# Optimization experiments

Measured on AMD Instinct MI355X. Metric: run time of the kernel, lower is better.

## Reference

```python
import jax, jax.numpy as jnp
import numpy as np

D_MODEL = 1024
N_HEADS = 16
D_HEAD = D_MODEL // N_HEADS  # 64
SCALE = 1.0 / float(np.sqrt(D_HEAD))


def setup_inputs() -> dict:
    key = jax.random.key(0)
    kx, kq, kk, kv, ko = jax.random.split(key, 5)
    B, L = 1, 4096
    x = jax.random.normal(kx, (B, L, D_MODEL), dtype=jnp.float32)
    init = 0.02  # small init so softmax isn't saturated
    Wq = jax.random.normal(kq, (D_MODEL, D_MODEL), dtype=jnp.float32) * init
    Wk = jax.random.normal(kk, (D_MODEL, D_MODEL), dtype=jnp.float32) * init
    Wv = jax.random.normal(kv, (D_MODEL, D_MODEL), dtype=jnp.float32) * init
    Wo = jax.random.normal(ko, (D_MODEL, D_MODEL), dtype=jnp.float32) * init
    return {"x": x, "Wq": Wq, "Wk": Wk, "Wv": Wv, "Wo": Wo}


def reference(x, Wq, Wk, Wv, Wo):
    # x: [B, L, d_model]; torch Linear (no bias): y = x @ W.T
    B, L, _ = x.shape

    def split_heads(t):  # [B, L, d_model] -> [B, H, L, Dh]
        return t.reshape(B, L, N_HEADS, D_HEAD).transpose(0, 2, 1, 3)

    q = split_heads(x @ Wq.T)
    k = split_heads(x @ Wk.T)
    v = split_heads(x @ Wv.T)

    # Full (non-flash) attention: explicit [B, H, L, L] scores (causal=False, eval dropout=0)
    scores = jnp.einsum("bhld,bhmd->bhlm", q, k) * SCALE
    attn = jax.nn.softmax(scores, axis=-1)
    out = jnp.einsum("bhlm,bhmd->bhld", attn, v)

    out = out.transpose(0, 2, 1, 3).reshape(B, L, D_MODEL)
    return out @ Wo.T
```

## Files before the change

### kernel.cpp

```cpp
#include <hip/hip_runtime.h>

typedef _Float16 f16_t;
typedef __fp16 fp16x2 __attribute__((ext_vector_type(2)));
typedef _Float16 f16x2 __attribute__((ext_vector_type(2)));
typedef _Float16 f16x4 __attribute__((ext_vector_type(4)));
typedef _Float16 f16x8 __attribute__((ext_vector_type(8)));
typedef float f32x4 __attribute__((ext_vector_type(4)));

#define D_MODEL 1024
#define LSEQ 4096
#define NH 16
#define DH 64
#define QSCALE 0.18033688011112042f

#define GLDS16(g, l)                                                     \
    __builtin_amdgcn_global_load_lds(                                    \
        (const __attribute__((address_space(1))) void*)(g),              \
        (__attribute__((address_space(3))) void*)(l), 16, 0, 0)

#define WAIT_VM(n) asm volatile("s_waitcnt vmcnt(" #n ")" ::: "memory")

__global__ __launch_bounds__(256) void cvt_all(const float* __restrict__ x,
                                               const float* __restrict__ w0,
                                               const float* __restrict__ w1,
                                               const float* __restrict__ w2,
                                               const float* __restrict__ w3,
                                               f16_t* __restrict__ xb,
                                               f16_t* __restrict__ wq) {
    const int id = blockIdx.x;
    const float* src;
    f16_t* dst;
    float scale = 1.f;
    int i;
    if (id < 4096) {
        src = x; dst = xb;
        i = (id * 256 + threadIdx.x) * 4;
    } else {
        const int r = id - 4096;
        const int q = r >> 10;
        src = (q == 0) ? w0 : (q == 1) ? w1 : (q == 2) ? w2 : w3;
        if (q == 0) scale = QSCALE;
        dst = wq + (size_t)q * (D_MODEL * D_MODEL);
        i = ((r & 1023) * 256 + threadIdx.x) * 4;
    }
    float4 v = *(const float4*)&src[i];
    alignas(8) f16_t o4[4] = {(f16_t)(v.x * scale), (f16_t)(v.y * scale),
                              (f16_t)(v.z * scale), (f16_t)(v.w * scale)};
    *(uint2*)&dst[i] = *(const uint2*)o4;
}

__global__ __launch_bounds__(256, 3) void gemm_f16(const f16_t* __restrict__ A,
                                                   const f16_t* __restrict__ B,
                                                   void* __restrict__ Cout,
                                                   int M, int N, int K, int mode) {
    __shared__ alignas(16) f16_t As[3][128 * 32];
    __shared__ alignas(16) f16_t Bs[3][128 * 32];

    const int tid  = threadIdx.x;
    const int wave = tid >> 6;
    const int lane = tid & 63;
    const int quad = lane >> 4;
    const int l16  = lane & 15;
    const int wm = (wave & 1) * 64;
    const int wn = (wave >> 1) * 64;

    const int gx  = gridDim.x;
    const int gy  = gridDim.y;
    const int lid = blockIdx.y * gx + blockIdx.x;
    const int xcd = lid & 7;
    const int sub = lid >> 3;
    const int bm  = (xcd * (gx >> 3) + sub / gy) * 128;
    const int bn  = (sub % gy) * 128;

    f32x4 acc[4][4] = {};
    const int nk = K / 32;

    auto stage = [&](int kt, int b) {
        const int c0 = wave * 2;
        GLDS16(&A[(size_t)(bm + c0 * 16 + l16) * K + kt * 32 + quad * 8],
               &As[b][c0 * 512]);
        GLDS16(&A[(size_t)(bm + (c0 + 1) * 16 + l16) * K + kt * 32 + quad * 8],
               &As[b][(c0 + 1) * 512]);
        GLDS16(&B[(size_t)(bn + c0 * 16 + l16) * K + kt * 32 + quad * 8],
               &Bs[b][c0 * 512]);
        GLDS16(&B[(size_t)(bn + (c0 + 1) * 16 + l16) * K + kt * 32 + quad * 8],
               &Bs[b][(c0 + 1) * 512]);
    };

    stage(0, 0);
    stage(1, 1);
    for (int kt = 0; kt < nk; ++kt) {
        const int cb = kt % 3;
        if (kt < nk - 1) WAIT_VM(4);
        else             WAIT_VM(0);
        __syncthreads();
        if (kt + 2 < nk) stage(kt + 2, (kt + 2) % 3);

        f16x8 af[4], bfr[4];
#pragma unroll
        for (int mt = 0; mt < 4; ++mt)
            af[mt] = *(const f16x8*)&As[cb][((wm >> 4) + mt) * 512 + lane * 8];
#pragma unroll
        for (int nt = 0; nt < 4; ++nt)
            bfr[nt] = *(const f16x8*)&Bs[cb][((wn >> 4) + nt) * 512 + lane * 8];
#pragma unroll
        for (int mt = 0; mt < 4; ++mt)
#pragma unroll
            for (int nt = 0; nt < 4; ++nt)
                acc[mt][nt] = __builtin_amdgcn_mfma_f32_16x16x32_f16(
                    bfr[nt], af[mt], acc[mt][nt], 0, 0, 0);
    }

#pragma unroll
    for (int mt = 0; mt < 4; ++mt)
#pragma unroll
        for (int nt = 0; nt < 4; ++nt) {
            int row = bm + wm + mt * 16 + l16;
            int col = bn + wn + nt * 16 + quad * 4;
            if (mode == 0) {
                f16x4 p = {(f16_t)acc[mt][nt][0], (f16_t)acc[mt][nt][1],
                           (f16_t)acc[mt][nt][2], (f16_t)acc[mt][nt][3]};
                *(f16x4*)&((f16_t*)Cout)[((size_t)(col >> 6) * M + row) * 64 +
                                         (col & 63)] = p;
            } else {
                *(f32x4*)&((float*)Cout)[(size_t)row * N + col] = acc[mt][nt];
            }
        }
}

__global__ __launch_bounds__(256) void transpose_v(const f16_t* __restrict__ vh,
                                                   f16_t* __restrict__ v4) {
    __shared__ f16_t Ts[64][72];
    const int t = threadIdx.x;
    const int lt = blockIdx.x;
    const int head = blockIdx.y;

#pragma unroll
    for (int i = 0; i < 2; ++i) {
        int idx = t + i * 256;
        int row = idx >> 3, part = idx & 7;
        *(uint4*)&Ts[row][part * 8] =
            *(const uint4*)&vh[((size_t)head * LSEQ + lt * 64 + row) * DH + part * 8];
    }
    __syncthreads();

    const int c8  = t >> 5;
    const int mtp = c8 >> 2, dt = c8 & 3;
    const int l0  = (t & 31) * 2;
    alignas(16) f16_t buf[16];
#pragma unroll
    for (int li = 0; li < 2; ++li) {
        const int l = l0 + li;
        const int g = l >> 4, l16 = l & 15;
#pragma unroll
        for (int j = 0; j < 8; ++j) {
            int key = mtp * 32 + (j < 4 ? 4 * g + j : 16 + 4 * g + (j - 4));
            buf[li * 8 + j] = Ts[key][dt * 16 + l16];
        }
    }
    f16_t* dst = v4 + (size_t)head * (LSEQ * DH) + (size_t)lt * 4096 + c8 * 512 + l0 * 8;
    *(uint4*)&dst[0] = *(const uint4*)&buf[0];
    *(uint4*)&dst[8] = *(const uint4*)&buf[8];
}

__global__ __launch_bounds__(512, 4) void attn_kernel(const f16_t* __restrict__ qh,
                                                      const f16_t* __restrict__ kh,
                                                      const f16_t* __restrict__ v4,
                                                      f16_t* __restrict__ ao) {
    __shared__ alignas(16) f16_t smem[32768];
    __shared__ alignas(16) float lscr[8 * 64];
    f16_t* KsB = smem;
    f16_t* VsB = smem + 16384;

    const int tid  = threadIdx.x;
    const int wave = tid >> 6;
    const int lane = tid & 63;
    const int quad = lane >> 4;
    const int l16  = lane & 15;
    const int wq   = wave & 3;
    const int kha  = wave >> 2;

    const int id = blockIdx.x;
    const int head = id & 15;
    const int qrow0 = (id >> 4) * 128 + wq * 32;

    const f16_t* Q  = qh + (size_t)head * LSEQ * DH;
    const f16_t* K  = kh + (size_t)head * LSEQ * DH;
    const f16_t* V4 = v4 + (size_t)head * (LSEQ * DH);

    f16x8 qf[2][2];
#pragma unroll
    for (int qt = 0; qt < 2; ++qt)
#pragma unroll
        for (int kc = 0; kc < 2; ++kc)
            qf[qt][kc] = *(const f16x8*)
                &Q[(size_t)(qrow0 + qt * 16 + l16) * DH + kc * 32 + quad * 8];

    f32x4 o[4][2] = {};
    float lp[2] = {0.f, 0.f};

    auto stage = [&](int kt, int b) {
        f16_t* ks = KsB + (kha * 2 + b) * 4096;
        f16_t* vs = VsB + (kha * 2 + b) * 4096;
        const int ktg = kha * 32 + kt;
#pragma unroll
        for (int jj = 0; jj < 2; ++jj) {
            const int j = wq * 2 + jj;
            GLDS16(&K[(size_t)(ktg * 64 + wq * 16 + l16) * DH + jj * 32 + quad * 8],
                   &ks[j * 512]);
            GLDS16(&V4[(size_t)ktg * 4096 + wq * 1024 + jj * 512 + lane * 8],
                   &vs[wq * 1024 + jj * 512]);
        }
    };

    const int NT = LSEQ / 2 / 64;
    stage(0, 0);
    for (int kt = 0; kt < NT; ++kt) {
        const int cb = kt & 1;
        WAIT_VM(0);
        __syncthreads();
        if (kt + 1 < NT) stage(kt + 1, cb ^ 1);

        const f16_t* ks = KsB + (kha * 2 + cb) * 4096;
        const f16_t* vs = VsB + (kha * 2 + cb) * 4096;

        f32x4 sA[2][2] = {};
        {
            f16x8 kfA[4];
#pragma unroll
            for (int c = 0; c < 4; ++c)
                kfA[c] = *(const f16x8*)&ks[c * 512 + lane * 8];
#pragma unroll
            for (int h = 0; h < 2; ++h)
#pragma unroll
                for (int qt = 0; qt < 2; ++qt) {
                    sA[h][qt] = __builtin_amdgcn_mfma_f32_16x16x32_f16(
                        kfA[h * 2 + 0], qf[qt][0], sA[h][qt], 0, 0, 0);
                    sA[h][qt] = __builtin_amdgcn_mfma_f32_16x16x32_f16(
                        kfA[h * 2 + 1], qf[qt][1], sA[h][qt], 0, 0, 0);
                }
        }
        f32x4 sB[2][2] = {};
        {
            f16x8 kfB[4];
#pragma unroll
            for (int c = 0; c < 4; ++c)
                kfB[c] = *(const f16x8*)&ks[(4 + c) * 512 + lane * 8];
#pragma unroll
            for (int h = 0; h < 2; ++h)
#pragma unroll
                for (int qt = 0; qt < 2; ++qt) {
                    sB[h][qt] = __builtin_amdgcn_mfma_f32_16x16x32_f16(
                        kfB[h * 2 + 0], qf[qt][0], sB[h][qt], 0, 0, 0);
                    sB[h][qt] = __builtin_amdgcn_mfma_f32_16x16x32_f16(
                        kfB[h * 2 + 1], qf[qt][1], sB[h][qt], 0, 0, 0);
                }
        }

#pragma unroll
        for (int mtp = 0; mtp < 2; ++mtp) {
            f32x4 (*s)[2] = (mtp == 0) ? sA : sB;

            f16x8 vfd[4];
#pragma unroll
            for (int dt = 0; dt < 4; ++dt)
                vfd[dt] = *(const f16x8*)&vs[(mtp * 4 + dt) * 512 + lane * 8];

#pragma unroll
            for (int qt = 0; qt < 2; ++qt) {
                float e0 = __builtin_amdgcn_exp2f(s[0][qt][0]);
                float e1 = __builtin_amdgcn_exp2f(s[0][qt][1]);
                float e2 = __builtin_amdgcn_exp2f(s[0][qt][2]);
                float e3 = __builtin_amdgcn_exp2f(s[0][qt][3]);
                float e4 = __builtin_amdgcn_exp2f(s[1][qt][0]);
                float e5 = __builtin_amdgcn_exp2f(s[1][qt][1]);
                float e6 = __builtin_amdgcn_exp2f(s[1][qt][2]);
                float e7 = __builtin_amdgcn_exp2f(s[1][qt][3]);
                lp[qt] += ((e0 + e1) + (e2 + e3)) + ((e4 + e5) + (e6 + e7));
                fp16x2 p01 = __builtin_amdgcn_cvt_pkrtz(e0, e1);
                fp16x2 p23 = __builtin_amdgcn_cvt_pkrtz(e2, e3);
                fp16x2 p45 = __builtin_amdgcn_cvt_pkrtz(e4, e5);
                fp16x2 p67 = __builtin_amdgcn_cvt_pkrtz(e6, e7);
                f16x8 p = {__builtin_bit_cast(f16x2, p01)[0],
                           __builtin_bit_cast(f16x2, p01)[1],
                           __builtin_bit_cast(f16x2, p23)[0],
                           __builtin_bit_cast(f16x2, p23)[1],
                           __builtin_bit_cast(f16x2, p45)[0],
                           __builtin_bit_cast(f16x2, p45)[1],
                           __builtin_bit_cast(f16x2, p67)[0],
                           __builtin_bit_cast(f16x2, p67)[1]};
#pragma unroll
                for (int dt = 0; dt < 4; ++dt)
                    o[dt][qt] = __builtin_amdgcn_mfma_f32_16x16x32_f16(
                        vfd[dt], p, o[dt][qt], 0, 0, 0);
            }
        }
    }

    __syncthreads();
    float* scr = (float*)smem;
    if (wave >= 4) {
#pragma unroll
        for (int dt = 0; dt < 4; ++dt)
#pragma unroll
            for (int qt = 0; qt < 2; ++qt)
                *(f32x4*)&scr[(((wave - 4) * 8 + dt * 2 + qt) * 64 + lane) * 4] =
                    o[dt][qt];
#pragma unroll
        for (int qt = 0; qt < 2; ++qt)
            lscr[((wave - 4) * 2 + qt) * 64 + lane] = lp[qt];
    }
    __syncthreads();
    if (wave < 4) {
#pragma unroll
        for (int dt = 0; dt < 4; ++dt)
#pragma unroll
            for (int qt = 0; qt < 2; ++qt)
                o[dt][qt] += *(const f32x4*)
                    &scr[((wave * 8 + dt * 2 + qt) * 64 + lane) * 4];
#pragma unroll
        for (int qt = 0; qt < 2; ++qt) {
            float t = lp[qt] + lscr[(wave * 2 + qt) * 64 + lane];
            t += __shfl_xor(t, 16, 64);
            t += __shfl_xor(t, 32, 64);
            lp[qt] = 1.f / t;
        }
#pragma unroll
        for (int dt = 0; dt < 4; ++dt)
#pragma unroll
            for (int qt = 0; qt < 2; ++qt) {
                f16x4 ov = {(f16_t)(o[dt][qt][0] * lp[qt]),
                            (f16_t)(o[dt][qt][1] * lp[qt]),
                            (f16_t)(o[dt][qt][2] * lp[qt]),
                            (f16_t)(o[dt][qt][3] * lp[qt])};
                int qrow = qrow0 + qt * 16 + l16;
                *(f16x4*)&ao[(size_t)qrow * D_MODEL + head * 64 + dt * 16 +
                             quad * 4] = ov;
            }
    }
}

extern "C" void kernel_launch(void* const* d_in, const int* in_sizes, int n_in,
                              void* d_out, int out_size, void* d_ws, size_t ws_size,
                              hipStream_t stream) {
    const float* x  = (const float*)d_in[0];
    const float* Wq = (const float*)d_in[1];
    const float* Wk = (const float*)d_in[2];
    const float* Wv = (const float*)d_in[3];
    const float* Wo = (const float*)d_in[4];

    f16_t* xb = (f16_t*)d_ws;
    f16_t* wq = xb + (size_t)LSEQ * D_MODEL;
    f16_t* wo = wq + (size_t)3 * D_MODEL * D_MODEL;
    f16_t* qh = wo + (size_t)D_MODEL * D_MODEL;
    f16_t* kh = qh + (size_t)LSEQ * D_MODEL;
    f16_t* vh = kh + (size_t)LSEQ * D_MODEL;
    f16_t* v4 = vh + (size_t)LSEQ * D_MODEL;
    f16_t* ao = v4 + (size_t)LSEQ * D_MODEL;

    cvt_all<<<4096 + 4 * 1024, 256, 0, stream>>>(x, Wq, Wk, Wv, Wo, xb, wq);

    gemm_f16<<<dim3(LSEQ / 128, 3 * D_MODEL / 128), 256, 0, stream>>>(
        xb, wq, qh, LSEQ, 3 * D_MODEL, D_MODEL, 0);

    transpose_v<<<dim3(LSEQ / 64, NH), 256, 0, stream>>>(vh, v4);

    attn_kernel<<<dim3((LSEQ / 128) * NH), 512, 0, stream>>>(qh, kh, v4, ao);

    gemm_f16<<<dim3(LSEQ / 128, D_MODEL / 128), 256, 0, stream>>>(
        ao, wo, d_out, LSEQ, D_MODEL, D_MODEL, 1);
}
```

Before: 245.2 us.

## Fuse V transpose into QKV GEMM epilogue and raise attention MFMA priority

The separate transpose_v kernel is removed. Blocks of the QKV GEMM that produce V columns now stage their tile in shared memory and write it straight into the MFMA-friendly v4 layout. This saves one kernel launch and a full read and write of V, at the cost of an extra LDS round trip and syncs in those blocks. The attention inner loop is also wrapped in s_setprio(1)/(0) to favour waves issuing MFMA work.

```diff
diff --git a/kernel.cpp b/kernel.cpp
--- a/kernel.cpp
+++ b/kernel.cpp
@@ -52,9 +52,9 @@
 __global__ __launch_bounds__(256, 3) void gemm_f16(const f16_t* __restrict__ A,
                                                    const f16_t* __restrict__ B,
                                                    void* __restrict__ Cout,
+                                                   f16_t* __restrict__ v4out,
                                                    int M, int N, int K, int mode) {
-    __shared__ alignas(16) f16_t As[3][128 * 32];
-    __shared__ alignas(16) f16_t Bs[3][128 * 32];
+    __shared__ alignas(16) f16_t sm[24576];
 
     const int tid  = threadIdx.x;
     const int wave = tid >> 6;
@@ -78,13 +78,13 @@
     auto stage = [&](int kt, int b) {
         const int c0 = wave * 2;
         GLDS16(&A[(size_t)(bm + c0 * 16 + l16) * K + kt * 32 + quad * 8],
-               &As[b][c0 * 512]);
+               &sm[b * 4096 + c0 * 512]);
         GLDS16(&A[(size_t)(bm + (c0 + 1) * 16 + l16) * K + kt * 32 + quad * 8],
-               &As[b][(c0 + 1) * 512]);
+               &sm[b * 4096 + (c0 + 1) * 512]);
         GLDS16(&B[(size_t)(bn + c0 * 16 + l16) * K + kt * 32 + quad * 8],
-               &Bs[b][c0 * 512]);
+               &sm[12288 + b * 4096 + c0 * 512]);
         GLDS16(&B[(size_t)(bn + (c0 + 1) * 16 + l16) * K + kt * 32 + quad * 8],
-               &Bs[b][(c0 + 1) * 512]);
+               &sm[12288 + b * 4096 + (c0 + 1) * 512]);
     };
 
     stage(0, 0);
@@ -99,10 +99,10 @@
         f16x8 af[4], bfr[4];
 #pragma unroll
         for (int mt = 0; mt < 4; ++mt)
-            af[mt] = *(const f16x8*)&As[cb][((wm >> 4) + mt) * 512 + lane * 8];
+            af[mt] = *(const f16x8*)&sm[cb * 4096 + ((wm >> 4) + mt) * 512 + lane * 8];
 #pragma unroll
         for (int nt = 0; nt < 4; ++nt)
-            bfr[nt] = *(const f16x8*)&Bs[cb][((wn >> 4) + nt) * 512 + lane * 8];
+            bfr[nt] = *(const f16x8*)&sm[12288 + cb * 4096 + ((wn >> 4) + nt) * 512 + lane * 8];
 #pragma unroll
         for (int mt = 0; mt < 4; ++mt)
 #pragma unroll
@@ -111,56 +111,51 @@
                     bfr[nt], af[mt], acc[mt][nt], 0, 0, 0);
     }
 
-#pragma unroll
-    for (int mt = 0; mt < 4; ++mt)
-#pragma unroll
-        for (int nt = 0; nt < 4; ++nt) {
-            int row = bm + wm + mt * 16 + l16;
-            int col = bn + wn + nt * 16 + quad * 4;
-            if (mode == 0) {
+    const bool isV = (mode == 0) && (bn >= 2 * D_MODEL);
+    if (!isV) {
+#pragma unroll
+        for (int mt = 0; mt < 4; ++mt)
+#pragma unroll
+            for (int nt = 0; nt < 4; ++nt) {
+                int row = bm + wm + mt * 16 + l16;
+                int col = bn + wn + nt * 16 + quad * 4;
+                if (mode == 0) {
+                    f16x4 p = {(f16_t)acc[mt][nt][0], (f16_t)acc[mt][nt][1],
+                               (f16_t)acc[mt][nt][2], (f16_t)acc[mt][nt][3]};
+                    *(f16x4*)&((f16_t*)Cout)[((size_t)(col >> 6) * M + row) * 64 +
+                                             (col & 63)] = p;
+                } else {
+                    *(f32x4*)&((float*)Cout)[(size_t)row * N + col] = acc[mt][nt];
+                }
+            }
+    } else {
+        __syncthreads();
+#pragma unroll
+        for (int mt = 0; mt < 4; ++mt)
+#pragma unroll
+            for (int nt = 0; nt < 4; ++nt) {
                 f16x4 p = {(f16_t)acc[mt][nt][0], (f16_t)acc[mt][nt][1],
                            (f16_t)acc[mt][nt][2], (f16_t)acc[mt][nt][3]};
-                *(f16x4*)&((f16_t*)Cout)[((size_t)(col >> 6) * M + row) * 64 +
-                                         (col & 63)] = p;
-            } else {
-                *(f32x4*)&((float*)Cout)[(size_t)row * N + col] = acc[mt][nt];
-            }
-        }
-}
-
-__global__ __launch_bounds__(256) void transpose_v(const f16_t* __restrict__ vh,
-                                                   f16_t* __restrict__ v4) {
-    __shared__ f16_t Ts[64][72];
-    const int t = threadIdx.x;
-    const int lt = blockIdx.x;
-    const int head = blockIdx.y;
-
-#pragma unroll
-    for (int i = 0; i < 2; ++i) {
-        int idx = t + i * 256;
-        int row = idx >> 3, part = idx & 7;
-        *(uint4*)&Ts[row][part * 8] =
-            *(const uint4*)&vh[((size_t)head * LSEQ + lt * 64 + row) * DH + part * 8];
-    }
-    __syncthreads();
-
-    const int c8  = t >> 5;
-    const int mtp = c8 >> 2, dt = c8 & 3;
-    const int l0  = (t & 31) * 2;
-    alignas(16) f16_t buf[16];
-#pragma unroll
-    for (int li = 0; li < 2; ++li) {
-        const int l = l0 + li;
-        const int g = l >> 4, l16 = l & 15;
-#pragma unroll
-        for (int j = 0; j < 8; ++j) {
-            int key = mtp * 32 + (j < 4 ? 4 * g + j : 16 + 4 * g + (j - 4));
-            buf[li * 8 + j] = Ts[key][dt * 16 + l16];
-        }
-    }
-    f16_t* dst = v4 + (size_t)head * (LSEQ * DH) + (size_t)lt * 4096 + c8 * 512 + l0 * 8;
-    *(uint4*)&dst[0] = *(const uint4*)&buf[0];
-    *(uint4*)&dst[8] = *(const uint4*)&buf[8];
+                *(f16x4*)&sm[(wm + mt * 16 + l16) * 136 + wn + nt * 16 + quad * 4] = p;
+            }
+        __syncthreads();
+        const int hh = wave >> 1, lt = wave & 1;
+        const int head = ((bn - 2 * D_MODEL) >> 6) + hh;
+        const int ltg  = (bm >> 6) + lt;
+        const int g = lane >> 4, l16f = lane & 15;
+        f16_t* dst = v4out + (size_t)head * (LSEQ * DH) + (size_t)ltg * 4096;
+#pragma unroll
+        for (int c8 = 0; c8 < 8; ++c8) {
+            const int mtp = c8 >> 2, dt = c8 & 3;
+            alignas(16) f16_t buf[8];
+#pragma unroll
+            for (int j = 0; j < 8; ++j) {
+                int key = lt * 64 + mtp * 32 + (j < 4 ? 4 * g + j : 16 + 4 * g + (j - 4));
+                buf[j] = sm[key * 136 + hh * 64 + dt * 16 + l16f];
+            }
+            *(uint4*)&dst[c8 * 512 + lane * 8] = *(const uint4*)buf;
+        }
+    }
 }
 
 __global__ __launch_bounds__(512, 4) void attn_kernel(const f16_t* __restrict__ qh,
@@ -224,6 +219,7 @@
         const f16_t* ks = KsB + (kha * 2 + cb) * 4096;
         const f16_t* vs = VsB + (kha * 2 + cb) * 4096;
 
+        __builtin_amdgcn_s_setprio(1);
         f32x4 sA[2][2] = {};
         {
             f16x8 kfA[4];
@@ -295,6 +291,7 @@
                         vfd[dt], p, o[dt][qt], 0, 0, 0);
             }
         }
+        __builtin_amdgcn_s_setprio(0);
     }
 
     __syncthreads();
@@ -361,12 +358,10 @@
     cvt_all<<<4096 + 4 * 1024, 256, 0, stream>>>(x, Wq, Wk, Wv, Wo, xb, wq);
 
     gemm_f16<<<dim3(LSEQ / 128, 3 * D_MODEL / 128), 256, 0, stream>>>(
-        xb, wq, qh, LSEQ, 3 * D_MODEL, D_MODEL, 0);
-
-    transpose_v<<<dim3(LSEQ / 64, NH), 256, 0, stream>>>(vh, v4);
+        xb, wq, qh, v4, LSEQ, 3 * D_MODEL, D_MODEL, 0);
 
     attn_kernel<<<dim3((LSEQ / 128) * NH), 512, 0, stream>>>(qh, kh, v4, ao);
 
     gemm_f16<<<dim3(LSEQ / 128, D_MODEL / 128), 256, 0, stream>>>(
-        ao, wo, d_out, LSEQ, D_MODEL, D_MODEL, 1);
+        ao, wo, d_out, v4, LSEQ, D_MODEL, D_MODEL, 1);
 }
```

Result: no change. 244.5 us (-0.3%).
